# Performance work log

Hardware: AMD Instinct MI355X
Metric: run time of the kernel (lower is better)

The kernel has to match this reference:

```python
import jax, jax.numpy as jnp
import numpy as np

B, D, M, C = 256, 256, 65536, 1000
TEMP = 0.05
ALPHA_WEIGHT = 0.5
EPS = 1e-6


def setup_inputs() -> dict:
    key = jax.random.key(0)
    k = jax.random.split(key, 6)
    feat = jax.random.normal(k[0], (B, D), dtype=jnp.float32)
    features = jax.random.normal(k[1], (M, D), dtype=jnp.float32)
    features = features / jnp.clip(jnp.linalg.norm(features, axis=1, keepdims=True), 1e-12)
    sample_softlabels = jax.random.uniform(k[2], (M, C), dtype=jnp.float32)
    indexes = jax.random.randint(k[3], (B,), 0, M, dtype=jnp.int32)
    labels = jax.random.randint(k[4], (M,), 0, C, dtype=jnp.int32)
    batch_indexs_labels = jax.random.randint(k[5], (B,), 0, M, dtype=jnp.int32)
    return {
        "feat": feat,
        "features": features,
        "sample_softlabels": sample_softlabels,
        "indexes": indexes,
        "labels": labels,
        "batch_indexs_labels": batch_indexs_labels,
        "cur_epoch": 1,
    }


def reference(feat, features, sample_softlabels, indexes, labels, batch_indexs_labels, cur_epoch):
    # L2-normalize batch features (F.normalize with eps clamp)
    x = feat / jnp.clip(jnp.linalg.norm(feat, axis=1, keepdims=True), 1e-12)
    # HM.apply forward: similarity vs memory bank (memory momentum update is a
    # buffer side-effect and does not affect the returned loss)
    logits = (x @ features.T) / TEMP  # [B, M]
    # group similarities by class label of each memory slot (index_add_)
    sim = jax.ops.segment_sum(logits.T, labels, num_segments=C)  # [C, B]
    nums = jax.ops.segment_sum(jnp.ones((M,), jnp.float32), labels, num_segments=C)  # [C]
    mask = nums > 0
    sim = sim / jnp.where(mask, nums, 1.0)[:, None]  # class-mean similarity [C, B]
    simT = sim.T  # [B, C]
    # masked softmax over classes
    exps = jnp.exp(simT) * mask[None, :].astype(simT.dtype)
    probs = exps / (jnp.sum(exps, axis=1, keepdims=True) + EPS)
    log_probs = jnp.log(probs + EPS)  # [B, C]
    targets = labels[indexes]  # [B]
    loss1 = -jnp.mean(log_probs[jnp.arange(B), targets])
    if cur_epoch == 0:
        return loss1
    batch_soft_labels = sample_softlabels[batch_indexs_labels]  # [B, C]
    loss2 = jnp.sum(jnp.mean(-batch_soft_labels * log_probs, axis=0))
    return ALPHA_WEIGHT * loss1 + (1.0 - ALPHA_WEIGHT) * loss2
```

## Files before the change

kernel.cpp:

```cpp
#include <hip/hip_runtime.h>

#define B_SZ 256
#define D_SZ 256
#define M_SZ 65536
#define C_SZ 1000
#define TEMP 0.05f
#define EPSF 1e-6f

#define CPB 2
#define NBLK_CSUM (C_SZ / CPB)
#define LCAP 512


#define OFF_FCT   0
#define OFF_NUMS  1024000
#define OFF_ACC   1028000
#define OFF_LCNT  1028008

__launch_bounds__(1024)
__global__ void k_csum(const float* __restrict__ features,
                       const int* __restrict__ labels,
                       float* __restrict__ fct, int* __restrict__ nums,
                       float* __restrict__ acc, int* __restrict__ lcnt) {
    __shared__ int list[CPB][LCAP];
    __shared__ int lcur[CPB];
    __shared__ float4 red[CPB][8][64];
    int t = threadIdx.x, b = blockIdx.x;
    int c0 = b * CPB;

    if (t < CPB) lcur[t] = 0;
    if (b == 0 && t == 0) { acc[0] = 0.f; acc[1] = 0.f; lcnt[0] = 0; }
    __syncthreads();

    const int4* L4 = (const int4*)labels;
    #pragma unroll
    for (int k = 0; k < M_SZ / 4 / 1024; ++k) {
        int idx = k * 1024 + t;
        int4 l4 = L4[idx];
        int m0 = idx * 4;
        unsigned d;
        d = (unsigned)(l4.x - c0); if (d < CPB) list[d][atomicAdd(&lcur[d], 1)] = m0 + 0;
        d = (unsigned)(l4.y - c0); if (d < CPB) list[d][atomicAdd(&lcur[d], 1)] = m0 + 1;
        d = (unsigned)(l4.z - c0); if (d < CPB) list[d][atomicAdd(&lcur[d], 1)] = m0 + 2;
        d = (unsigned)(l4.w - c0); if (d < CPB) list[d][atomicAdd(&lcur[d], 1)] = m0 + 3;
    }
    __syncthreads();

    int g = t >> 9;
    int tt = t & 511;
    int s = tt >> 6;
    int lane = tt & 63;
    int c = c0 + g;
    int n = lcur[g];
    const int* ml = list[g];
    float4 a = make_float4(0.f, 0.f, 0.f, 0.f);
    #pragma unroll 2
    for (int i = s; i < n; i += 8) {
        float4 v = *(const float4*)&features[(size_t)ml[i] * D_SZ + lane * 4];
        a.x += v.x; a.y += v.y; a.z += v.z; a.w += v.w;
    }
    red[g][s][lane] = a;
    __syncthreads();
    if (s == 0) {
        float4 z = make_float4(0.f, 0.f, 0.f, 0.f);
        #pragma unroll
        for (int q = 0; q < 8; ++q) {
            float4 r = red[g][q][lane];
            z.x += r.x; z.y += r.y; z.z += r.z; z.w += r.w;
        }
        float scale = 1.0f / (TEMP * (float)(n > 0 ? n : 1));
        z.x *= scale; z.y *= scale; z.z *= scale; z.w *= scale;
        *(float4*)&fct[(size_t)lane * (C_SZ * 4) + c * 4] = z;
        if (lane == 0) nums[c] = n;
    }
}

__launch_bounds__(1024)
__global__ void k_loss(const float* __restrict__ feat,
                       const float* __restrict__ fct,
                       const int* __restrict__ nums,
                       const float* __restrict__ soft,
                       const int* __restrict__ indexes,
                       const int* __restrict__ labels,
                       const int* __restrict__ bil,
                       const int* __restrict__ cur_epoch,
                       float* __restrict__ acc, int* __restrict__ lcnt,
                       float* __restrict__ out) {
    __shared__ float xs0[D_SZ], xs1[D_SZ];
    __shared__ float wred[16], wred2[16];
    __shared__ float bc0, bc1;
    __shared__ int tgt0, tgt1, sr0, sr1;

    int t = threadIdx.x;
    int lane = t & 63, wid = t >> 6;
    int r0 = blockIdx.x * 2;

    if (t == 0) {
        tgt0 = labels[indexes[r0]];
        tgt1 = labels[indexes[r0 + 1]];
        sr0 = bil[r0];
        sr1 = bil[r0 + 1];
    }

    float v = (t < 512) ? feat[(size_t)r0 * D_SZ + t] : 0.f;
    float s = v * v;
    #pragma unroll
    for (int o = 32; o; o >>= 1) s += __shfl_down(s, o);
    if (lane == 0) wred[wid] = s;
    __syncthreads();
    if (t == 0) {
        bc0 = fmaxf(sqrtf(wred[0] + wred[1] + wred[2] + wred[3]), 1e-12f);
        bc1 = fmaxf(sqrtf(wred[4] + wred[5] + wred[6] + wred[7]), 1e-12f);
    }
    __syncthreads();
    if (t < 256) xs0[t] = v / bc0;
    else if (t < 512) xs1[t - 256] = v / bc1;
    __syncthreads();

    float a0 = 0.f, a1 = 0.f;
    if (t < C_SZ) {
        const float4* F = (const float4*)fct;
        #pragma unroll 4
        for (int j = 0; j < D_SZ / 4; ++j) {
            float4 f4 = F[(size_t)j * C_SZ + t];
            float4 x0 = *(const float4*)&xs0[4 * j];
            float4 x1 = *(const float4*)&xs1[4 * j];
            a0 = fmaf(x0.x, f4.x, a0); a0 = fmaf(x0.y, f4.y, a0);
            a0 = fmaf(x0.z, f4.z, a0); a0 = fmaf(x0.w, f4.w, a0);
            a1 = fmaf(x1.x, f4.x, a1); a1 = fmaf(x1.y, f4.y, a1);
            a1 = fmaf(x1.z, f4.z, a1); a1 = fmaf(x1.w, f4.w, a1);
        }
    }
    float mk = (t < C_SZ && nums[t] > 0) ? 1.f : 0.f;
    float e0 = mk * __expf(a0);
    float e1 = mk * __expf(a1);

    float s0 = e0, s1 = e1;
    #pragma unroll
    for (int o = 32; o; o >>= 1) {
        s0 += __shfl_down(s0, o);
        s1 += __shfl_down(s1, o);
    }
    if (lane == 0) { wred[wid] = s0; wred2[wid] = s1; }
    __syncthreads();
    if (t == 0) {
        float z0 = 0.f, z1 = 0.f;
        #pragma unroll
        for (int i = 0; i < 16; ++i) { z0 += wred[i]; z1 += wred2[i]; }
        bc0 = z0; bc1 = z1;
    }
    __syncthreads();
    float inv0 = 1.0f / (bc0 + EPSF);
    float inv1 = 1.0f / (bc1 + EPSF);

    float p1 = 0.f, p2 = 0.f;
    if (t < C_SZ) {
        float lp0 = __logf(e0 * inv0 + EPSF);
        float lp1 = __logf(e1 * inv1 + EPSF);
        p2 = -(soft[(size_t)sr0 * C_SZ + t] * lp0 + soft[(size_t)sr1 * C_SZ + t] * lp1);
        if (t == tgt0) p1 -= lp0;
        if (t == tgt1) p1 -= lp1;
    }
    #pragma unroll
    for (int o = 32; o; o >>= 1) {
        p1 += __shfl_down(p1, o);
        p2 += __shfl_down(p2, o);
    }
    __syncthreads();
    if (lane == 0) { wred[wid] = p1; wred2[wid] = p2; }
    __syncthreads();
    if (t == 0) {
        float z1 = 0.f, z2 = 0.f;
        #pragma unroll
        for (int i = 0; i < 16; ++i) { z1 += wred[i]; z2 += wred2[i]; }
        atomicAdd(&acc[0], z1);
        atomicAdd(&acc[1], z2);
        __threadfence();
        int done = atomicAdd(lcnt, 1);
        if (done == (int)gridDim.x - 1) {
            float l1 = atomicAdd(&acc[0], 0.f) / (float)B_SZ;
            float l2 = atomicAdd(&acc[1], 0.f) / (float)B_SZ;
            out[0] = (cur_epoch[0] == 0) ? l1 : 0.5f * (l1 + l2);
        }
    }
}

extern "C" void kernel_launch(void* const* d_in, const int* in_sizes, int n_in,
                              void* d_out, int out_size, void* d_ws, size_t ws_size,
                              hipStream_t stream) {
    const float* feat     = (const float*)d_in[0];
    const float* features = (const float*)d_in[1];
    const float* soft     = (const float*)d_in[2];
    const int* indexes    = (const int*)d_in[3];
    const int* labels     = (const int*)d_in[4];
    const int* bil        = (const int*)d_in[5];
    const int* cur_epoch  = (const int*)d_in[6];

    char* ws = (char*)d_ws;
    float* fct   = (float*)(ws + OFF_FCT);
    int* nums    = (int*)(ws + OFF_NUMS);
    float* acc   = (float*)(ws + OFF_ACC);
    int* lcnt    = (int*)(ws + OFF_LCNT);

    k_csum<<<NBLK_CSUM, 1024, 0, stream>>>(features, labels, fct, nums, acc, lcnt);
    k_loss<<<B_SZ / 2, 1024, 0, stream>>>(feat, fct, nums, soft, indexes, labels,
                                          bil, cur_epoch, acc, lcnt, (float*)d_out);
}
```

Baseline: 41.41 us.

## Restructure loss kernel to one row per block with split-K class tiles

The loss kernel now uses one batch row per block (256 blocks instead of 128). Each thread computes four classes over a quarter of the feature dimension, and the four partial sums are reduced through shared memory. This spreads the small class-similarity GEMV across more blocks and threads to raise occupancy and give wider per-thread loads. The trade-off is that the class-feature matrix is read once per row instead of once per row pair, and there is an extra shared-memory reduction. The class-sum gather loop unroll is also raised from 2 to 8.

```diff
diff --git a/kernel.cpp b/kernel.cpp
--- a/kernel.cpp
+++ b/kernel.cpp
@@ -54,7 +54,7 @@
     int n = lcur[g];
     const int* ml = list[g];
     float4 a = make_float4(0.f, 0.f, 0.f, 0.f);
-    #pragma unroll 2
+    #pragma unroll 8
     for (int i = s; i < n; i += 8) {
         float4 v = *(const float4*)&features[(size_t)ml[i] * D_SZ + lane * 4];
         a.x += v.x; a.y += v.y; a.z += v.z; a.w += v.w;
@@ -86,80 +86,97 @@
                        const int* __restrict__ cur_epoch,
                        float* __restrict__ acc, int* __restrict__ lcnt,
                        float* __restrict__ out) {
-    __shared__ float xs0[D_SZ], xs1[D_SZ];
+    __shared__ float xs[D_SZ];
+    __shared__ float pa[4][256][5];
     __shared__ float wred[16], wred2[16];
-    __shared__ float bc0, bc1;
-    __shared__ int tgt0, tgt1, sr0, sr1;
+    __shared__ float bc0;
+    __shared__ int tgt0, sr0;
 
     int t = threadIdx.x;
     int lane = t & 63, wid = t >> 6;
-    int r0 = blockIdx.x * 2;
+    int r = blockIdx.x;
 
     if (t == 0) {
-        tgt0 = labels[indexes[r0]];
-        tgt1 = labels[indexes[r0 + 1]];
-        sr0 = bil[r0];
-        sr1 = bil[r0 + 1];
-    }
-
-    float v = (t < 512) ? feat[(size_t)r0 * D_SZ + t] : 0.f;
+        tgt0 = labels[indexes[r]];
+        sr0 = bil[r];
+    }
+
+    float v = (t < D_SZ) ? feat[(size_t)r * D_SZ + t] : 0.f;
     float s = v * v;
     #pragma unroll
     for (int o = 32; o; o >>= 1) s += __shfl_down(s, o);
     if (lane == 0) wred[wid] = s;
     __syncthreads();
+    if (t == 0)
+        bc0 = fmaxf(sqrtf(wred[0] + wred[1] + wred[2] + wred[3]), 1e-12f);
+    __syncthreads();
+    if (t < D_SZ) xs[t] = v / bc0;
+    __syncthreads();
+
+    int q = t >> 8, tt = t & 255;
+    int c0 = 4 * tt;
+    float b0 = 0.f, b1 = 0.f, b2 = 0.f, b3 = 0.f;
+    if (tt < 250) {
+        int jb = q * 16;
+        #pragma unroll 4
+        for (int j = jb; j < jb + 16; ++j) {
+            const float* base = fct + (size_t)j * (C_SZ * 4) + c0 * 4;
+            float4 f0 = *(const float4*)(base);
+            float4 f1 = *(const float4*)(base + 4);
+            float4 f2 = *(const float4*)(base + 8);
+            float4 f3 = *(const float4*)(base + 12);
+            float4 x = *(const float4*)&xs[4 * j];
+            b0 = fmaf(x.x, f0.x, b0); b0 = fmaf(x.y, f0.y, b0);
+            b0 = fmaf(x.z, f0.z, b0); b0 = fmaf(x.w, f0.w, b0);
+            b1 = fmaf(x.x, f1.x, b1); b1 = fmaf(x.y, f1.y, b1);
+            b1 = fmaf(x.z, f1.z, b1); b1 = fmaf(x.w, f1.w, b1);
+            b2 = fmaf(x.x, f2.x, b2); b2 = fmaf(x.y, f2.y, b2);
+            b2 = fmaf(x.z, f2.z, b2); b2 = fmaf(x.w, f2.w, b2);
+            b3 = fmaf(x.x, f3.x, b3); b3 = fmaf(x.y, f3.y, b3);
+            b3 = fmaf(x.z, f3.z, b3); b3 = fmaf(x.w, f3.w, b3);
+        }
+    }
+    pa[q][tt][0] = b0; pa[q][tt][1] = b1;
+    pa[q][tt][2] = b2; pa[q][tt][3] = b3;
+    __syncthreads();
+
+    float e0[4] = {0.f, 0.f, 0.f, 0.f};
+    float s0 = 0.f;
+    if (t < 250) {
+        int4 nm = *(const int4*)&nums[4 * t];
+        #pragma unroll
+        for (int k = 0; k < 4; ++k) {
+            float a0 = (pa[0][t][k] + pa[1][t][k]) + (pa[2][t][k] + pa[3][t][k]);
+            int nk = (k == 0) ? nm.x : (k == 1) ? nm.y : (k == 2) ? nm.z : nm.w;
+            float mk = (nk > 0) ? 1.f : 0.f;
+            e0[k] = mk * __expf(a0);
+            s0 += e0[k];
+        }
+    }
+    #pragma unroll
+    for (int o = 32; o; o >>= 1) s0 += __shfl_down(s0, o);
+    if (lane == 0) wred[wid] = s0;
+    __syncthreads();
     if (t == 0) {
-        bc0 = fmaxf(sqrtf(wred[0] + wred[1] + wred[2] + wred[3]), 1e-12f);
-        bc1 = fmaxf(sqrtf(wred[4] + wred[5] + wred[6] + wred[7]), 1e-12f);
-    }
-    __syncthreads();
-    if (t < 256) xs0[t] = v / bc0;
-    else if (t < 512) xs1[t - 256] = v / bc1;
-    __syncthreads();
-
-    float a0 = 0.f, a1 = 0.f;
-    if (t < C_SZ) {
-        const float4* F = (const float4*)fct;
-        #pragma unroll 4
-        for (int j = 0; j < D_SZ / 4; ++j) {
-            float4 f4 = F[(size_t)j * C_SZ + t];
-            float4 x0 = *(const float4*)&xs0[4 * j];
-            float4 x1 = *(const float4*)&xs1[4 * j];
-            a0 = fmaf(x0.x, f4.x, a0); a0 = fmaf(x0.y, f4.y, a0);
-            a0 = fmaf(x0.z, f4.z, a0); a0 = fmaf(x0.w, f4.w, a0);
-            a1 = fmaf(x1.x, f4.x, a1); a1 = fmaf(x1.y, f4.y, a1);
-            a1 = fmaf(x1.z, f4.z, a1); a1 = fmaf(x1.w, f4.w, a1);
-        }
-    }
-    float mk = (t < C_SZ && nums[t] > 0) ? 1.f : 0.f;
-    float e0 = mk * __expf(a0);
-    float e1 = mk * __expf(a1);
-
-    float s0 = e0, s1 = e1;
-    #pragma unroll
-    for (int o = 32; o; o >>= 1) {
-        s0 += __shfl_down(s0, o);
-        s1 += __shfl_down(s1, o);
-    }
-    if (lane == 0) { wred[wid] = s0; wred2[wid] = s1; }
-    __syncthreads();
-    if (t == 0) {
-        float z0 = 0.f, z1 = 0.f;
-        #pragma unroll
-        for (int i = 0; i < 16; ++i) { z0 += wred[i]; z1 += wred2[i]; }
-        bc0 = z0; bc1 = z1;
+        float z0 = 0.f;
+        #pragma unroll
+        for (int i = 0; i < 16; ++i) z0 += wred[i];
+        bc0 = z0;
     }
     __syncthreads();
     float inv0 = 1.0f / (bc0 + EPSF);
-    float inv1 = 1.0f / (bc1 + EPSF);
 
     float p1 = 0.f, p2 = 0.f;
-    if (t < C_SZ) {
-        float lp0 = __logf(e0 * inv0 + EPSF);
-        float lp1 = __logf(e1 * inv1 + EPSF);
-        p2 = -(soft[(size_t)sr0 * C_SZ + t] * lp0 + soft[(size_t)sr1 * C_SZ + t] * lp1);
-        if (t == tgt0) p1 -= lp0;
-        if (t == tgt1) p1 -= lp1;
+    if (t < 250) {
+        int c0b = 4 * t;
+        float4 sp0 = *(const float4*)&soft[(size_t)sr0 * C_SZ + c0b];
+        #pragma unroll
+        for (int k = 0; k < 4; ++k) {
+            float w0 = (k == 0) ? sp0.x : (k == 1) ? sp0.y : (k == 2) ? sp0.z : sp0.w;
+            float lp0 = __logf(e0[k] * inv0 + EPSF);
+            p2 -= w0 * lp0;
+            if (c0b + k == tgt0) p1 -= lp0;
+        }
     }
     #pragma unroll
     for (int o = 32; o; o >>= 1) {
@@ -203,6 +220,6 @@
     int* lcnt    = (int*)(ws + OFF_LCNT);
 
     k_csum<<<NBLK_CSUM, 1024, 0, stream>>>(features, labels, fct, nums, acc, lcnt);
-    k_loss<<<B_SZ / 2, 1024, 0, stream>>>(feat, fct, nums, soft, indexes, labels,
-                                          bil, cur_epoch, acc, lcnt, (float*)d_out);
+    k_loss<<<B_SZ, 1024, 0, stream>>>(feat, fct, nums, soft, indexes, labels,
+                                      bil, cur_epoch, acc, lcnt, (float*)d_out);
 }
```

Measured after the change: 54.37 us. +31.3%, slower.
